# Kernel optimization log

Measured on AMD Instinct MI355X. Metric: run time of the kernel, lower is better.

Reference implementation:

```python
import jax, jax.numpy as jnp
import numpy as np

N_INST = 8  # max instance id; ids 1..N_INST, 0 = background
MESH_NORM = 1024.0  # from SegmantationLoss._meshgrid


def _meshgrid(H, W):
    y = jnp.arange(H, dtype=jnp.float32) / MESH_NORM
    x = jnp.arange(W, dtype=jnp.float32) / MESH_NORM
    return jnp.stack([jnp.broadcast_to(y[:, None], (H, W)),
                      jnp.broadcast_to(x[None, :], (H, W))], axis=0)  # [2,H,W]


def _lovasz_hinge_batch(logits, labels, delta=1.0):
    """logits, labels: [K,P] float. Returns [K] lovasz hinge losses."""
    signs = 2.0 * labels - 1.0
    errors = delta - logits * signs
    order = jnp.argsort(-errors, axis=1)  # descending
    es = jnp.take_along_axis(errors, order, axis=1)
    gs = jnp.take_along_axis(labels, order, axis=1)
    gts = gs.sum(axis=1, keepdims=True)
    intersection = gts - jnp.cumsum(gs, axis=1)
    union = gts + jnp.cumsum(1.0 - gs, axis=1)
    jac = 1.0 - intersection / union
    grad = jnp.concatenate([jac[:, :1], jac[:, 1:] - jac[:, :-1]], axis=1)
    return (jax.nn.relu(es) * grad).sum(axis=1)


def setup_inputs() -> dict:
    key = jax.random.key(0)
    k1, k2, k3, k4 = jax.random.split(key, 4)
    B, H, W = 4, 512, 1024
    x_vec = jax.random.normal(k1, (B, 2, H, W), dtype=jnp.float32)
    # small scale so psigma = exp(10*ppsigma) stays in a sane range
    x_sigma = jax.random.normal(k2, (B, 2, H, W), dtype=jnp.float32) * 0.03
    x_seed = jax.random.normal(k3, (B, 1, H, W), dtype=jnp.float32)
    t = jax.random.randint(k4, (B, H, W), 0, 9, dtype=jnp.int32)
    return {"x_vec": x_vec, "x_sigma": x_sigma, "x_seed": x_seed, "t": t}


def reference(x_vec, x_sigma, x_seed, t):
    B, _, H, W = x_vec.shape
    mesh = _meshgrid(H, W)

    emb = jnp.tanh(x_vec) + mesh[None]          # [B,2,H,W] spatial embedding
    ppsig = x_sigma                              # [B,2,H,W] pre-pseudo-sigma
    seed = jax.nn.sigmoid(x_seed)[:, 0]          # [B,H,W]

    ids = jnp.arange(1, N_INST + 1, dtype=t.dtype)
    mf = (t[None] == ids[:, None, None, None]).astype(jnp.float32)  # [N,B,H,W]
    cnt = mf.sum(axis=(2, 3))                    # [N,B]
    present = cnt > 0
    safe = jnp.maximum(cnt, 1.0)
    n_present = jnp.maximum(present.sum(axis=0).astype(jnp.float32), 1.0)  # [B]

    # per-instance masked means
    centroid = jnp.einsum('nbhw,bchw->nbc', mf, emb) / safe[..., None]    # [N,B,2]
    inst_pps = jnp.einsum('nbhw,bchw->nbc', mf, ppsig) / safe[..., None]  # [N,B,2]
    psigma = jnp.exp(10.0 * inst_pps)                                     # [N,B,2]

    # gaussian between pixel and instance embedding (l22n)
    diff2 = (emb[None] - centroid[..., None, None]) ** 2                  # [N,B,2,H,W]
    dist = (diff2 * psigma[..., None, None]).sum(axis=2)                  # [N,B,H,W]
    gauss = jnp.exp(-0.5 * dist)                                          # [N,B,H,W]

    # lovasz hinge per instance on logits 2*gauss - 1 over all pixels
    P = H * W
    lov = _lovasz_hinge_batch((2.0 * gauss - 1.0).reshape(N_INST * B, P),
                              mf.reshape(N_INST * B, P)).reshape(N_INST, B)
    lov = jnp.where(present, lov, 0.0)
    lovasz_loss = (lov.sum(axis=0) / n_present).mean()

    # sigma loss: pixel ppsigma -> detached instance mean ppsigma
    sd = (ppsig[None] - jax.lax.stop_gradient(inst_pps)[..., None, None]) ** 2
    sl = (sd.sum(axis=2) * mf).sum(axis=(2, 3)) / safe                    # [N,B]
    sl = jnp.where(present, sl, 0.0)
    sigma_loss = (sl.sum(axis=0) / n_present).mean()

    # seed loss: background -> 0, foreground -> detached gaussian
    bg = (t == 0).astype(jnp.float32)                                     # [B,H,W]
    bg_cnt = jnp.maximum(bg.sum(axis=(1, 2)), 1.0)
    bg_loss = ((seed ** 2) * bg).sum(axis=(1, 2)) / bg_cnt                # [B]
    fg = ((seed[None] - jax.lax.stop_gradient(gauss)) ** 2 * mf).sum(axis=(2, 3)) / safe
    fg = jnp.where(present, fg, 0.0)
    seed_loss = ((bg_loss + fg.sum(axis=0)) /
                 (1.0 + present.sum(axis=0).astype(jnp.float32))).mean()

    return lovasz_loss + sigma_loss + seed_loss
```

## Files before the change

### kernel.cpp

```cpp
#include <hip/hip_runtime.h>
#include <math.h>

#define B 4
#define H 512
#define W 1024
#define P (H*W)
#define NI 8
#define NSEG 32
#define NB 512
#define INV_BW ((float)NB/2.0f)
#define NSTRIP 128
#define STRIP_PX (P/NSTRIP)
#define K1B 128
#define K1PX (P/K1B)

#define D_CENY 0
#define D_CENX 32
#define D_PSY  64
#define D_PSX  96
#define D_CNT  128
#define D_SL   160
#define D_K4C  192
#define OFF_FGP 256
#define OFF_HIST (256 + 9*512)
#define OFF_FOLD (OFF_HIST + NSEG*NSTRIP*NB)
#define OFF_PK1  OFF_HIST

__device__ __forceinline__ float fast_tanh(float x) {
    float e = __expf(2.0f * x);
    return 1.0f - 2.0f / (e + 1.0f);
}
__device__ __forceinline__ float fast_sigmoid(float x) {
    return 1.0f / (1.0f + __expf(-x));
}
template<int CTRL, int RM>
__device__ __forceinline__ float dpp_add(float x) {
    int y = __builtin_amdgcn_update_dpp(0, __float_as_int(x), CTRL, RM, 0xF, true);
    return x + __int_as_float(y);
}
__device__ __forceinline__ float wred(float x) {
    x = dpp_add<0x111, 0xF>(x);
    x = dpp_add<0x112, 0xF>(x);
    x = dpp_add<0x114, 0xF>(x);
    x = dpp_add<0x118, 0xF>(x);
    x = dpp_add<0x142, 0xA>(x);
    x = dpp_add<0x143, 0xC>(x);
    return x;
}

__global__ __launch_bounds__(256) void k1_stats(const float* __restrict__ xv,
                                                const float* __restrict__ xs,
                                                const int*  __restrict__ t,
                                                float* __restrict__ pk1) {
    const int b = blockIdx.y, bx = blockIdx.x, tid = threadIdx.x;
    const int lane = tid & 63, wid = tid >> 6;
    const float* xv_y = xv + (size_t)b*2*P;
    const float* xv_x = xv_y + P;
    const float* xs_y = xs + (size_t)b*2*P;
    const float* xs_x = xs_y + P;
    const int*   tb   = t + (size_t)b*P;

    float cnt[NI], sey[NI], sex[NI], sgy[NI], sgx[NI], sq[NI];
    #pragma unroll
    for (int n = 0; n < NI; ++n) { cnt[n]=0.f; sey[n]=0.f; sex[n]=0.f; sgy[n]=0.f; sgx[n]=0.f; sq[n]=0.f; }

    #pragma unroll
    for (int it = 0; it < 4; ++it) {
        int p0 = bx*K1PX + it*1024 + tid*4;
        float4 vy = *(const float4*)(xv_y + p0);
        float4 vx = *(const float4*)(xv_x + p0);
        float4 sy = *(const float4*)(xs_y + p0);
        float4 sx = *(const float4*)(xs_x + p0);
        int4   tt = *(const int4*)(tb + p0);
        #pragma unroll
        for (int j = 0; j < 4; ++j) {
            int pix = p0 + j;
            float ey = fast_tanh((&vy.x)[j]) + (float)(pix >> 10) * (1.0f/1024.0f);
            float ex = fast_tanh((&vx.x)[j]) + (float)(pix & 1023) * (1.0f/1024.0f);
            float gy = (&sy.x)[j], gx = (&sx.x)[j];
            int tv = (&tt.x)[j];
            float q = gy*gy + gx*gx;
            #pragma unroll
            for (int n = 0; n < NI; ++n) {
                float m = (tv == n+1) ? 1.0f : 0.0f;
                cnt[n] += m; sey[n] += m*ey; sex[n] += m*ex;
                sgy[n] += m*gy; sgx[n] += m*gx; sq[n] += m*q;
            }
        }
    }
    __shared__ float sw[4*64];
    #define RED48(val, slot) { float r_ = wred(val); if (lane == 63) sw[wid*64 + (slot)] = r_; }
    #pragma unroll
    for (int n = 0; n < NI; ++n) {
        RED48(cnt[n], n*6+0); RED48(sey[n], n*6+1); RED48(sex[n], n*6+2);
        RED48(sgy[n], n*6+3); RED48(sgx[n], n*6+4); RED48(sq[n],  n*6+5);
    }
    #undef RED48
    __syncthreads();
    if (tid < 48) {
        float s = sw[tid] + sw[64+tid] + sw[128+tid] + sw[192+tid];
        pk1[(size_t)(b*K1B + bx)*64 + tid] = s;
    }
}

__global__ __launch_bounds__(1024) void k2_finalize(float* __restrict__ wsf,
                                                    const float* __restrict__ pk1,
                                                    float* __restrict__ out) {
    const int tid = threadIdx.x;
    __shared__ float part[16*64];
    __shared__ float ssum[4*64];
    const int v = tid & 63, g = tid >> 6;
    const int b = g >> 2, c = g & 3;
    float acc = 0.f;
    const int jbase = b*K1B + c*32;
    #pragma unroll 8
    for (int i = 0; i < 32; ++i) acc += pk1[(size_t)(jbase + i)*64 + v];
    part[g*64 + v] = acc;
    __syncthreads();
    if (tid < 256) {
        int vb = tid & 63, bb = tid >> 6;
        ssum[bb*64+vb] = part[(bb*4+0)*64+vb] + part[(bb*4+1)*64+vb]
                       + part[(bb*4+2)*64+vb] + part[(bb*4+3)*64+vb];
    }
    __syncthreads();
    if (tid < NSEG) {
        int n = tid >> 2, bb = tid & 3;
        float cv  = ssum[bb*64 + n*6+0];
        float sey = ssum[bb*64 + n*6+1];
        float sex = ssum[bb*64 + n*6+2];
        float sgy = ssum[bb*64 + n*6+3];
        float sgx = ssum[bb*64 + n*6+4];
        float sq  = ssum[bb*64 + n*6+5];
        float safe = fmaxf(cv, 1.0f);
        float ipy = sgy/safe, ipx = sgx/safe;
        wsf[D_CENY+tid] = sey/safe;
        wsf[D_CENX+tid] = sex/safe;
        wsf[D_PSY+tid]  = expf(10.0f*ipy);
        wsf[D_PSX+tid]  = expf(10.0f*ipx);
        wsf[D_CNT+tid]  = cv;
        wsf[D_SL+tid]   = sq/safe - (ipy*ipy + ipx*ipx);
    } else if (tid < 64) {
        ((unsigned*)wsf)[D_K4C + (tid - 32)] = 0u;
    } else if (tid == 64) {
        out[0] = 0.f;
    }
}

__global__ __launch_bounds__(512) void k3_hist(const float* __restrict__ xv,
                                               const float* __restrict__ xseed,
                                               const int*  __restrict__ t,
                                               const float* __restrict__ wsf,
                                               unsigned* __restrict__ hist_g,
                                               float* __restrict__ fgp) {
    const int strip = blockIdx.x;
    const int b     = blockIdx.y;
    const int tid   = threadIdx.x;
    const int lane  = tid & 63;

    __shared__ unsigned hist[NI*NB];
    {
        uint4 z = {0u,0u,0u,0u};
        #pragma unroll
        for (int i = 0; i < 2; ++i) *((uint4*)hist + i*512 + tid) = z;
    }
    __shared__ float spar[4*NI];
    if (tid < 4*NI) {
        int n = tid & (NI-1), q = tid >> 3;
        spar[tid] = wsf[q*32 + n*B + b];
    }
    __syncthreads();

    float ceny[NI], cenx[NI], psy[NI], psx[NI], fgn[NI];
    #pragma unroll
    for (int n = 0; n < NI; ++n) {
        ceny[n] = spar[n]; cenx[n] = spar[NI+n];
        psy[n] = spar[2*NI+n]; psx[n] = spar[3*NI+n];
        fgn[n] = 0.f;
    }
    float bgq = 0.f;

    const float* xv_y = xv + (size_t)b*2*P;
    const float* xv_x = xv_y + P;
    const float* sdp  = xseed + (size_t)b*P;
    const int*   tb   = t + (size_t)b*P;
    const int base = strip * STRIP_PX;

    #pragma unroll
    for (int it = 0; it < STRIP_PX/2048; ++it) {
        int p0 = base + it*2048 + tid*4;
        float4 vy = *(const float4*)(xv_y + p0);
        float4 vx = *(const float4*)(xv_x + p0);
        float4 se = *(const float4*)(sdp + p0);
        int4   tt = *(const int4*)(tb + p0);
        #pragma unroll
        for (int j = 0; j < 4; ++j) {
            int pix = p0 + j;
            float ey = fast_tanh((&vy.x)[j]) + (float)(pix >> 10) * (1.0f/1024.0f);
            float ex = fast_tanh((&vx.x)[j]) + (float)(pix & 1023) * (1.0f/1024.0f);
            int tv = (&tt.x)[j];
            float gown = 0.f;
            #pragma unroll
            for (int n = 0; n < NI; ++n) {
                float dy = ey - ceny[n], dx = ex - cenx[n];
                float g = __expf(-0.5f * (psy[n]*dy*dy + psx[n]*dx*dx));
                bool lab = (tv == n+1);
                float err = lab ? (2.0f - 2.0f*g) : (2.0f*g);
                int key = (int)(err * INV_BW);
                key = key > (NB-1) ? (NB-1) : key;
                if (key > 0) atomicAdd(&hist[n*NB + key], lab ? 0x10000u : 1u);
                if (lab) gown = g;
            }
            float s = fast_sigmoid((&se.x)[j]);
            if (tv > 0) {
                float d = s - gown;
                float dd = d*d;
                #pragma unroll
                for (int n = 0; n < NI; ++n) fgn[n] += (tv == n+1) ? dd : 0.f;
            } else {
                bgq += s*s;
            }
        }
    }
    __syncthreads();
    #pragma unroll
    for (int i = 0; i < 2; ++i) {
        int lin = i*2048 + tid*4;
        int n = lin >> 9, key = lin & (NB-1);
        uint4 v = *(const uint4*)&hist[lin];
        *(uint4*)&hist_g[((size_t)((n*4 + b)*NSTRIP + strip))*NB + key] = v;
    }
    __shared__ float sfg[NI+1];
    if (tid < NI+1) sfg[tid] = 0.f;
    __syncthreads();
    #pragma unroll
    for (int n = 0; n < NI; ++n) {
        float r = wred(fgn[n]);
        if (lane == 63 && r != 0.f) atomicAdd(&sfg[n], r);
    }
    {
        float r = wred(bgq);
        if (lane == 63) atomicAdd(&sfg[NI], r);
    }
    __syncthreads();
    if (tid < NI+1) fgp[tid*512 + b*NSTRIP + strip] = sfg[tid];
}

__global__ __launch_bounds__(256) void k4_fused(const unsigned* __restrict__ hist_g,
                                                unsigned* __restrict__ fold,
                                                float* __restrict__ wsf,
                                                const float* __restrict__ fgp,
                                                float* __restrict__ out) {
    const int q = blockIdx.x;
    const int seg = blockIdx.y;
    const int tid = threadIdx.x;

    #pragma unroll
    for (int h = 0; h < 2; ++h) {
        int key = h*256 + tid;
        const unsigned* src = hist_g + (size_t)(seg*NSTRIP + q*32)*NB + key;
        unsigned pos = 0u, neg = 0u;
        #pragma unroll 8
        for (int s = 0; s < 32; ++s) {
            unsigned v = src[(size_t)s*NB];
            pos += v >> 16; neg += v & 0xffffu;
        }
        fold[((size_t)q*NSEG + seg)*NB + key] = pos;
        fold[(size_t)4*NSEG*NB + ((size_t)q*NSEG + seg)*NB + key] = neg;
    }

    __shared__ unsigned slast;
    __syncthreads();
    if (tid == 0) {
        __threadfence();
        unsigned* cnt4 = (unsigned*)wsf + D_K4C;
        slast = __hip_atomic_fetch_add(&cnt4[seg], 1u, __ATOMIC_ACQ_REL,
                                       __HIP_MEMORY_SCOPE_AGENT);
    }
    __syncthreads();
    if (slast != 3u) return;
    __threadfence();

    const int n = seg >> 2, b = seg & 3;
    __shared__ float scnt[NSEG];
    __shared__ float sfr[128];
    __shared__ unsigned up[256], un[256];
    __shared__ double sdd[256];
    if (tid < NSEG) scnt[tid] = wsf[D_CNT + tid];
    __syncthreads();

    if (n == 0) {
        if (tid < 128) sfr[tid] = fgp[NI*512 + b*NSTRIP + tid];
        __syncthreads();
        #pragma unroll
        for (int d = 64; d > 0; d >>= 1) {
            if (tid < d) sfr[tid] += sfr[tid + d];
            __syncthreads();
        }
        if (tid == 0) {
            float bgs = sfr[0];
            int np = 0; float ss = 0.f, csum = 0.f;
            for (int k = 0; k < NI; ++k) {
                float cv = scnt[k*4 + b];
                csum += cv;
                if (cv > 0.5f) { np++; ss += wsf[D_SL + k*4 + b]; }
            }
            float bgc = fmaxf((float)P - csum, 1.0f);
            float bgl = bgs / bgc;
            float npf = fmaxf((float)np, 1.0f);
            atomicAdd(out, (ss/npf + bgl/(1.0f + (float)np)) * (1.0f/(float)B));
        }
        __syncthreads();
    }

    const float G = scnt[seg];
    if (G < 0.5f) return;
    int npc = 0;
    #pragma unroll
    for (int k = 0; k < NI; ++k) npc += (scnt[k*4 + b] > 0.5f) ? 1 : 0;

    if (tid < 128) sfr[tid] = fgp[n*512 + b*NSTRIP + tid];
    __syncthreads();
    #pragma unroll
    for (int d = 64; d > 0; d >>= 1) {
        if (tid < d) sfr[tid] += sfr[tid + d];
        __syncthreads();
    }
    const float FG = sfr[0];

    unsigned pos2[2] = {0u,0u}, neg2[2] = {0u,0u};
    #pragma unroll
    for (int qq = 0; qq < 4; ++qq) {
        uint2 pv = *((const uint2*)(fold + ((size_t)qq*NSEG + seg)*NB) + tid);
        uint2 nv = *((const uint2*)(fold + (size_t)4*NSEG*NB + ((size_t)qq*NSEG + seg)*NB) + tid);
        pos2[0] += pv.x; pos2[1] += pv.y;
        neg2[0] += nv.x; neg2[1] += nv.y;
    }
    unsigned tp = pos2[0] + pos2[1];
    unsigned tn = neg2[0] + neg2[1];

    up[tid] = tp; un[tid] = tn;
    __syncthreads();
    for (int d = 1; d < 256; d <<= 1) {
        unsigned ap = (tid + d < 256) ? up[tid + d] : 0u;
        unsigned an = (tid + d < 256) ? un[tid + d] : 0u;
        __syncthreads();
        up[tid] += ap; un[tid] += an;
        __syncthreads();
    }
    const unsigned TP = up[0], TN = un[0];
    const unsigned Gu = (unsigned)(G + 0.5f);
    const unsigned NEGu = (unsigned)P - Gu;
    unsigned cump = up[tid] - tp;
    unsigned cumn = un[tid] - tn;

    const double dG = (double)G;
    double acc = 0.0;
    #pragma unroll
    for (int j = 1; j >= 0; --j) {
        unsigned cp = pos2[j], cn = neg2[j];
        int key = tid*2 + j;
        if (tid == 0 && j == 0) { cp = Gu - TP; cn = NEGu - TN; }
        if (cp | cn) {
            unsigned ep = cump, en = cumn;
            unsigned epi = ep + cp, eni = en + cn;
            double jb = 1.0 - (dG - (double)ep)  / (dG + (double)en);
            double ja = 1.0 - (dG - (double)epi) / (dG + (double)eni);
            acc += (((double)key + 0.5) * (2.0/(double)NB)) * (ja - jb);
        }
        cump += cp; cumn += cn;
    }
    sdd[tid] = acc;
    __syncthreads();
    #pragma unroll
    for (int d = 128; d > 0; d >>= 1) {
        if (tid < d) sdd[tid] += sdd[tid + d];
        __syncthreads();
    }
    if (tid == 0) {
        float npf = fmaxf((float)npc, 1.0f);
        float val = (float)sdd[0] / (npf * (float)B)
                  + (FG / G) / ((1.0f + (float)npc) * (float)B);
        atomicAdd(out, val);
    }
}

extern "C" void kernel_launch(void* const* d_in, const int* in_sizes, int n_in,
                              void* d_out, int out_size, void* d_ws, size_t ws_size,
                              hipStream_t stream) {
    (void)in_sizes; (void)n_in; (void)out_size; (void)ws_size;
    const float* xv  = (const float*)d_in[0];
    const float* xs  = (const float*)d_in[1];
    const float* xsd = (const float*)d_in[2];
    const int*   t   = (const int*)d_in[3];
    float* wsf = (float*)d_ws;
    unsigned* hist_g = (unsigned*)d_ws + OFF_HIST;
    unsigned* fold   = (unsigned*)d_ws + OFF_FOLD;
    float* pk1 = wsf + OFF_PK1;
    float* fgp = wsf + OFF_FGP;
    float* out = (float*)d_out;

    k1_stats<<<dim3(K1B, B), 256, 0, stream>>>(xv, xs, t, pk1);
    k2_finalize<<<1, 1024, 0, stream>>>(wsf, pk1, out);
    k3_hist<<<dim3(NSTRIP, B), 512, 0, stream>>>(xv, xsd, t, wsf, hist_g, fgp);
    k4_fused<<<dim3(4, NSEG), 256, 0, stream>>>(hist_g, fold, wsf, fgp, out);
}
```

Measured before the change: 128.0 us.

## Split histogram kernel across instance groups and double stats-kernel grid

The histogram kernel now launches a third grid dimension that splits the 8 instances into two groups of 4, so each block builds a 4-instance shared histogram with fewer registers and less shared memory. The intent is more blocks and more occupancy for the dominant exp/atomic work. In exchange, each pixel's tanh embedding, seed and label loads are computed twice. The stats kernel also doubles its block count, halving the pixels per block, and the finalize reduction is adjusted to sum 64 partials per group.

```diff
diff --git a/kernel.cpp b/kernel.cpp
--- a/kernel.cpp
+++ b/kernel.cpp
@@ -11,7 +11,7 @@
 #define INV_BW ((float)NB/2.0f)
 #define NSTRIP 128
 #define STRIP_PX (P/NSTRIP)
-#define K1B 128
+#define K1B 256
 #define K1PX (P/K1B)
 
 #define D_CENY 0
@@ -65,7 +65,7 @@
     for (int n = 0; n < NI; ++n) { cnt[n]=0.f; sey[n]=0.f; sex[n]=0.f; sgy[n]=0.f; sgx[n]=0.f; sq[n]=0.f; }
 
     #pragma unroll
-    for (int it = 0; it < 4; ++it) {
+    for (int it = 0; it < 2; ++it) {
         int p0 = bx*K1PX + it*1024 + tid*4;
         float4 vy = *(const float4*)(xv_y + p0);
         float4 vx = *(const float4*)(xv_x + p0);
@@ -112,9 +112,9 @@
     const int v = tid & 63, g = tid >> 6;
     const int b = g >> 2, c = g & 3;
     float acc = 0.f;
-    const int jbase = b*K1B + c*32;
+    const int jbase = b*K1B + c*64;
     #pragma unroll 8
-    for (int i = 0; i < 32; ++i) acc += pk1[(size_t)(jbase + i)*64 + v];
+    for (int i = 0; i < 64; ++i) acc += pk1[(size_t)(jbase + i)*64 + v];
     part[g*64 + v] = acc;
     __syncthreads();
     if (tid < 256) {
@@ -154,28 +154,26 @@
                                                float* __restrict__ fgp) {
     const int strip = blockIdx.x;
     const int b     = blockIdx.y;
+    const int ng    = blockIdx.z;
+    const int n0    = ng*4;
     const int tid   = threadIdx.x;
     const int lane  = tid & 63;
 
-    __shared__ unsigned hist[NI*NB];
-    {
-        uint4 z = {0u,0u,0u,0u};
-        #pragma unroll
-        for (int i = 0; i < 2; ++i) *((uint4*)hist + i*512 + tid) = z;
-    }
-    __shared__ float spar[4*NI];
-    if (tid < 4*NI) {
-        int n = tid & (NI-1), q = tid >> 3;
-        spar[tid] = wsf[q*32 + n*B + b];
-    }
-    __syncthreads();
-
-    float ceny[NI], cenx[NI], psy[NI], psx[NI], fgn[NI];
-    #pragma unroll
-    for (int n = 0; n < NI; ++n) {
-        ceny[n] = spar[n]; cenx[n] = spar[NI+n];
-        psy[n] = spar[2*NI+n]; psx[n] = spar[3*NI+n];
-        fgn[n] = 0.f;
+    __shared__ unsigned hist[4*NB];
+    *((uint4*)hist + tid) = (uint4){0u,0u,0u,0u};
+    __shared__ float spar[16];
+    if (tid < 16) {
+        int gi = tid & 3, q = tid >> 2;
+        spar[tid] = wsf[q*32 + (n0 + gi)*B + b];
+    }
+    __syncthreads();
+
+    float ceny[4], cenx[4], psy[4], psx[4], fgn[4];
+    #pragma unroll
+    for (int gi = 0; gi < 4; ++gi) {
+        ceny[gi] = spar[gi]; cenx[gi] = spar[4+gi];
+        psy[gi] = spar[8+gi]; psx[gi] = spar[12+gi];
+        fgn[gi] = 0.f;
     }
     float bgq = 0.f;
 
@@ -200,49 +198,49 @@
             int tv = (&tt.x)[j];
             float gown = 0.f;
             #pragma unroll
-            for (int n = 0; n < NI; ++n) {
-                float dy = ey - ceny[n], dx = ex - cenx[n];
-                float g = __expf(-0.5f * (psy[n]*dy*dy + psx[n]*dx*dx));
-                bool lab = (tv == n+1);
+            for (int gi = 0; gi < 4; ++gi) {
+                float dy = ey - ceny[gi], dx = ex - cenx[gi];
+                float g = __expf(-0.5f * (psy[gi]*dy*dy + psx[gi]*dx*dx));
+                bool lab = (tv == n0 + gi + 1);
                 float err = lab ? (2.0f - 2.0f*g) : (2.0f*g);
                 int key = (int)(err * INV_BW);
                 key = key > (NB-1) ? (NB-1) : key;
-                if (key > 0) atomicAdd(&hist[n*NB + key], lab ? 0x10000u : 1u);
+                if (key > 0) atomicAdd(&hist[gi*NB + key], lab ? 0x10000u : 1u);
                 if (lab) gown = g;
             }
             float s = fast_sigmoid((&se.x)[j]);
-            if (tv > 0) {
+            if (tv > n0 && tv <= n0 + 4) {
                 float d = s - gown;
                 float dd = d*d;
                 #pragma unroll
-                for (int n = 0; n < NI; ++n) fgn[n] += (tv == n+1) ? dd : 0.f;
-            } else {
+                for (int gi = 0; gi < 4; ++gi) fgn[gi] += (tv == n0+gi+1) ? dd : 0.f;
+            } else if (ng == 0 && tv == 0) {
                 bgq += s*s;
             }
         }
     }
     __syncthreads();
-    #pragma unroll
-    for (int i = 0; i < 2; ++i) {
-        int lin = i*2048 + tid*4;
-        int n = lin >> 9, key = lin & (NB-1);
+    {
+        int lin = tid*4;
+        int gi = lin >> 9, key = lin & (NB-1);
         uint4 v = *(const uint4*)&hist[lin];
-        *(uint4*)&hist_g[((size_t)((n*4 + b)*NSTRIP + strip))*NB + key] = v;
-    }
-    __shared__ float sfg[NI+1];
-    if (tid < NI+1) sfg[tid] = 0.f;
-    __syncthreads();
-    #pragma unroll
-    for (int n = 0; n < NI; ++n) {
-        float r = wred(fgn[n]);
-        if (lane == 63 && r != 0.f) atomicAdd(&sfg[n], r);
-    }
-    {
+        *(uint4*)&hist_g[((size_t)(((n0+gi)*4 + b)*NSTRIP + strip))*NB + key] = v;
+    }
+    __shared__ float sfg[5];
+    if (tid < 5) sfg[tid] = 0.f;
+    __syncthreads();
+    #pragma unroll
+    for (int gi = 0; gi < 4; ++gi) {
+        float r = wred(fgn[gi]);
+        if (lane == 63 && r != 0.f) atomicAdd(&sfg[gi], r);
+    }
+    if (ng == 0) {
         float r = wred(bgq);
-        if (lane == 63) atomicAdd(&sfg[NI], r);
-    }
-    __syncthreads();
-    if (tid < NI+1) fgp[tid*512 + b*NSTRIP + strip] = sfg[tid];
+        if (lane == 63) atomicAdd(&sfg[4], r);
+    }
+    __syncthreads();
+    if (tid < 4) fgp[(n0 + tid)*512 + b*NSTRIP + strip] = sfg[tid];
+    else if (tid == 4 && ng == 0) fgp[NI*512 + b*NSTRIP + strip] = sfg[4];
 }
 
 __global__ __launch_bounds__(256) void k4_fused(const unsigned* __restrict__ hist_g,
@@ -401,6 +399,6 @@
 
     k1_stats<<<dim3(K1B, B), 256, 0, stream>>>(xv, xs, t, pk1);
     k2_finalize<<<1, 1024, 0, stream>>>(wsf, pk1, out);
-    k3_hist<<<dim3(NSTRIP, B), 512, 0, stream>>>(xv, xsd, t, wsf, hist_g, fgp);
+    k3_hist<<<dim3(NSTRIP, B, 2), 512, 0, stream>>>(xv, xsd, t, wsf, hist_g, fgp);
     k4_fused<<<dim3(4, NSEG), 256, 0, stream>>>(hist_g, fold, wsf, fgp, out);
 }
```

Measured after the change: 132.0 us. +3.1%, slower.
